# Kernel tuning notes

Hardware: AMD Instinct MI355X
Metric: run time of the kernel (lower is better)

## Reference

```python
import jax, jax.numpy as jnp
import numpy as np

D_IN = 1024
D_OUT = 1024


def setup_inputs() -> dict:
    key = jax.random.key(0)
    kx, kq, kk, kv = jax.random.split(key, 4)
    x = jax.random.normal(kx, (4, 2048, D_IN), dtype=jnp.float32)
    # nn.Linear weight has shape [d_out, d_in]; y = x @ W.T
    s = 1.0 / np.sqrt(D_IN)
    W_query = jax.random.uniform(kq, (D_OUT, D_IN), jnp.float32, -s, s)
    W_key = jax.random.uniform(kk, (D_OUT, D_IN), jnp.float32, -s, s)
    W_value = jax.random.uniform(kv, (D_OUT, D_IN), jnp.float32, -s, s)
    return {"x": x, "W_query": W_query, "W_key": W_key, "W_value": W_value}


def reference(x, W_query, W_key, W_value):
    # x: [b, n, d_in]; W_*: [d_out, d_in]
    q = jnp.einsum("bnd,kd->bnk", x, W_query)
    k = jnp.einsum("bnd,kd->bnk", x, W_key)
    v = jnp.einsum("bnd,kd->bnk", x, W_value)
    d_k = W_query.shape[0]
    scores = jnp.einsum("bqk,bnk->bqn", q, k) * (d_k ** -0.5)  # [b, n, n]
    weights = jax.nn.softmax(scores, axis=-1)
    return jnp.einsum("bqn,bnk->bqk", weights, v)
```

## Files before the change

kernel.cpp:

```cpp
#include <hip/hip_runtime.h>
#include <hip/hip_bf16.h>
#include <stdint.h>


typedef __attribute__((ext_vector_type(8))) short bf16x8;
typedef __attribute__((ext_vector_type(4))) float f32x4;

__device__ __forceinline__ void async_copy16(const void* g, void* l) {
  __builtin_amdgcn_global_load_lds(
      (__attribute__((address_space(1))) void*)(g),
      (__attribute__((address_space(3))) void*)(l),
      16, 0, 0);
}

template<int NI, int NT, int KS>
__device__ __forceinline__ void mainloop256(
    const __hip_bfloat16* __restrict__ aS,
    const __hip_bfloat16* __restrict__ bS,
    __hip_bfloat16* As, __hip_bfloat16* Bs,
    const int wid, const int wm, const int wn,
    const int l16, const int quad, const int sw,
    f32x4 (&acc)[8][NI])
{
  constexpr int NI2 = NI / 2;
  const bf16x8* Av = (const bf16x8*)As;
  const bf16x8* Bv = (const bf16x8*)Bs;
  char* lA = (char*)As + wid * 1024;
  char* lB = (char*)Bs + wid * 1024;
  bf16x8 bfr[NI][2];
  bf16x8 afc[2][2], afn[2][2];

#define SB0 __builtin_amdgcn_sched_barrier(0)

#define STG_A2(t) do { \
    _Pragma("unroll") \
    for (int p = 0; p < 4; ++p) \
      async_copy16(aS + ((t)*64 + (long long)p * 64 * KS), \
                   lA + ((t)&1)*32768 + p * 64 * 128); \
  } while (0)
#define STG_B2(t) do { \
    _Pragma("unroll") \
    for (int p = 0; p < NI; ++p) \
      async_copy16(bS + ((t)*64 + (long long)p * 64 * KS), \
                   lB + ((t)&1)*(NI*8192) + p * 64 * 128); \
  } while (0)

#define RD_AF(dst, t, phi) do { \
    _Pragma("unroll") \
    for (int m2 = 0; m2 < 2; ++m2) \
      _Pragma("unroll") \
      for (int kk = 0; kk < 2; ++kk) \
        dst[m2][kk] = Av[((t)&1)*2048 + (wm + ((phi)*2 + m2)*16 + l16)*8 + ((kk*4 + quad) ^ sw)]; \
  } while (0)
#define RD_BF(t, nlo, nhi) do { \
    _Pragma("unroll") \
    for (int ni = (nlo); ni < (nhi); ++ni) \
      _Pragma("unroll") \
      for (int kk = 0; kk < 2; ++kk) \
        bfr[ni][kk] = Bv[((t)&1)*(NI*512) + (wn + ni*16 + l16)*8 + ((kk*4 + quad) ^ sw)]; \
  } while (0)
#define MM(src, phi, nlo, nhi) do { \
    _Pragma("unroll") \
    for (int kk = 0; kk < 2; ++kk) \
      _Pragma("unroll") \
      for (int m2 = 0; m2 < 2; ++m2) \
        _Pragma("unroll") \
        for (int ni = (nlo); ni < (nhi); ++ni) \
          acc[(phi)*2 + m2][ni] = __builtin_amdgcn_mfma_f32_16x16x32_bf16( \
              src[m2][kk], bfr[ni][kk], acc[(phi)*2 + m2][ni], 0, 0, 0); \
  } while (0)

#define TILE(t, STG0_STMT, STG1_STMT, GATE_STMT) do { \
     \
    RD_BF(t, 0, NI2); \
    RD_AF(afc, t, 0); \
    STG0_STMT; \
    asm volatile("s_waitcnt lgkmcnt(0)"); SB0; \
    RD_BF(t, NI2, NI); \
    SB0; \
    RD_AF(afn, t, 1); \
    SB0; \
    __builtin_amdgcn_s_setprio(1); MM(afc, 0, 0, NI2); __builtin_amdgcn_s_setprio(0); \
    asm volatile("s_waitcnt lgkmcnt(4)"); SB0; \
    __builtin_amdgcn_s_setprio(1); MM(afc, 0, NI2, NI); __builtin_amdgcn_s_setprio(0); \
    SB0; \
    __builtin_amdgcn_s_barrier();    \
     \
    STG1_STMT; \
    asm volatile("s_waitcnt lgkmcnt(0)"); SB0; \
    RD_AF(afc, t, 2); \
    SB0; \
    __builtin_amdgcn_s_setprio(1); MM(afn, 1, 0, NI); __builtin_amdgcn_s_setprio(0); \
     \
    asm volatile("s_waitcnt lgkmcnt(0)"); SB0; \
    RD_AF(afn, t, 3); \
    SB0; \
    __builtin_amdgcn_s_setprio(1); MM(afc, 2, 0, NI); __builtin_amdgcn_s_setprio(0); \
     \
    asm volatile("s_waitcnt lgkmcnt(0)"); SB0; \
    __builtin_amdgcn_s_setprio(1); MM(afn, 3, 0, NI); __builtin_amdgcn_s_setprio(0); \
    GATE_STMT; \
    SB0; \
    __builtin_amdgcn_s_barrier(); \
  } while (0)

#define GATEN do { if constexpr (NI == 4) asm volatile("s_waitcnt vmcnt(4)"); \
                   else                   asm volatile("s_waitcnt vmcnt(2)"); } while (0)
#define GATE0 asm volatile("s_waitcnt vmcnt(0)")
#define GNONE (void)0

  STG_B2(0); STG_A2(0); STG_B2(1);
  GATEN;
  __builtin_amdgcn_s_barrier();

  #pragma unroll 1
  for (int i = 0; i < NT / 2 - 1; ++i) {
    const int ta = 2 * i, tb = 2 * i + 1;
    TILE(ta, STG_A2(tb),     STG_B2(ta + 2), GATEN);
    TILE(tb, STG_A2(ta + 2), STG_B2(tb + 2), GATEN);
  }
  TILE(NT - 2, STG_A2(NT - 1), GNONE, GATE0);
  TILE(NT - 1, GNONE,          GNONE, GNONE);

#undef TILE
#undef GATEN
#undef GATE0
#undef GNONE
#undef MM
#undef RD_BF
#undef RD_AF
#undef STG_A2
#undef STG_B2
#undef SB0
}

__global__ __launch_bounds__(512, 2)
void gemm_qk(const __hip_bfloat16* __restrict__ A,
             const __hip_bfloat16* __restrict__ B,
             __hip_bfloat16* __restrict__ Q,
             __hip_bfloat16* __restrict__ Kk)
{
  __shared__ __align__(16) __hip_bfloat16 As[2][256 * 64];
  __shared__ __align__(16) __hip_bfloat16 Bs[2][256 * 64];

  const int bid = blockIdx.x;
  const int s   = (bid & 7) * 32 + (bid >> 3);
  const long long tile_m = (long long)(s >> 3) * 256;
  const long long tile_n = (long long)(s & 7) * 256;

  const int tid  = threadIdx.x;
  const int wid  = tid >> 6;
  const int lane = tid & 63;
  const int srow = wid * 8 + (lane >> 3);
  const int scol = ((lane & 7) ^ (lane >> 3)) * 8;

  const __hip_bfloat16* aS = A + (tile_m + srow) * 1024 + scol;
  const __hip_bfloat16* bS = B + (tile_n + srow) * 1024 + scol;

  const int wm   = (wid >> 2) * 128;
  const int wn   = (wid & 3) * 64;
  const int quad = lane >> 4;
  const int l16  = lane & 15;
  const int sw   = l16 & 7;

  f32x4 acc[8][4];
  #pragma unroll
  for (int mi = 0; mi < 8; ++mi)
    #pragma unroll
    for (int ni = 0; ni < 4; ++ni)
      acc[mi][ni] = (f32x4){0.f, 0.f, 0.f, 0.f};

  mainloop256<4, 16, 1024>(aS, bS, &As[0][0], &Bs[0][0],
                           wid, wm, wn, l16, quad, sw, acc);

  const int mat = (int)(tile_n >> 10);
  __hip_bfloat16* outp = (mat == 0) ? Q : Kk;
  const float scale = (mat == 0) ? 0.03125f : 1.0f;
  const int coln0 = (int)(tile_n & 1023);
  #pragma unroll
  for (int mi = 0; mi < 8; ++mi) {
    #pragma unroll
    for (int r = 0; r < 4; ++r) {
      const long long row = tile_m + wm + mi * 16 + quad * 4 + r;
      #pragma unroll
      for (int ni = 0; ni < 4; ++ni) {
        const int col = coln0 + wn + ni * 16 + l16;
        outp[row * 1024 + col] = __float2bfloat16(acc[mi][ni][r] * scale);
      }
    }
  }
}

__global__ __launch_bounds__(512, 2)
void gemm_v(const __hip_bfloat16* __restrict__ A,
            const __hip_bfloat16* __restrict__ B,
            __hip_bfloat16* __restrict__ Vt)
{
  __shared__ __align__(16) __hip_bfloat16 As[2][256 * 64];
  __shared__ __align__(16) __hip_bfloat16 Bs[2][128 * 64];

  const int bid = blockIdx.x;
  const int s   = (bid & 7) * 32 + (bid >> 3);
  const long long tile_m = (long long)(s >> 3) * 256;
  const long long tile_n = (long long)(s & 7) * 128;

  const int tid  = threadIdx.x;
  const int wid  = tid >> 6;
  const int lane = tid & 63;
  const int srow = wid * 8 + (lane >> 3);
  const int scol = ((lane & 7) ^ (lane >> 3)) * 8;

  const __hip_bfloat16* aS = A + (tile_m + srow) * 1024 + scol;
  const __hip_bfloat16* bS = B + (tile_n + srow) * 1024 + scol;

  const int wm   = (wid >> 2) * 128;
  const int wn   = (wid & 3) * 32;
  const int quad = lane >> 4;
  const int l16  = lane & 15;
  const int sw   = l16 & 7;

  f32x4 acc[8][2];
  #pragma unroll
  for (int mi = 0; mi < 8; ++mi)
    #pragma unroll
    for (int ni = 0; ni < 2; ++ni)
      acc[mi][ni] = (f32x4){0.f, 0.f, 0.f, 0.f};

  mainloop256<2, 16, 1024>(aS, bS, &As[0][0], &Bs[0][0],
                           wid, wm, wn, l16, quad, sw, acc);

  const int b    = (int)(tile_m >> 11);
  const int seq0 = (int)(tile_m & 2047);
  const int d0   = (int)tile_n;
  #pragma unroll
  for (int mi = 0; mi < 8; ++mi) {
    const int seq = seq0 + wm + mi * 16 + quad * 4;
    #pragma unroll
    for (int ni = 0; ni < 2; ++ni) {
      const int d = d0 + wn + ni * 16 + l16;
      union { ushort4 u; unsigned short sh[4]; } pk;
      #pragma unroll
      for (int r = 0; r < 4; ++r)
        pk.sh[r] = __bfloat16_as_ushort(__float2bfloat16(acc[mi][ni][r]));
      *(ushort4*)(Vt + ((long long)(b * 1024 + d)) * 2048 + seq) = pk.u;
    }
  }
}

__global__ __launch_bounds__(512, 2)
void gemm_s_exp(const __hip_bfloat16* __restrict__ A,
                const __hip_bfloat16* __restrict__ B,
                __hip_bfloat16* __restrict__ Cout,
                float* __restrict__ part)
{
  __shared__ __align__(16) __hip_bfloat16 As[2][256 * 64];
  __shared__ __align__(16) __hip_bfloat16 Bs[2][256 * 64];

  const int bz = blockIdx.z;
  A += (long long)bz * 2048 * 1024;
  B += (long long)bz * 2048 * 1024;

  const long long tile_m = (long long)blockIdx.y * 256;
  const long long tile_n = (long long)blockIdx.x * 256;

  const int tid  = threadIdx.x;
  const int wid  = tid >> 6;
  const int lane = tid & 63;
  const int srow = wid * 8 + (lane >> 3);
  const int scol = ((lane & 7) ^ (lane >> 3)) * 8;

  const __hip_bfloat16* aS = A + (tile_m + srow) * 1024 + scol;
  const __hip_bfloat16* bS = B + (tile_n + srow) * 1024 + scol;

  const int wm   = (wid >> 2) * 128;
  const int wn   = (wid & 3) * 64;
  const int quad = lane >> 4;
  const int l16  = lane & 15;
  const int sw   = l16 & 7;

  f32x4 acc[8][4];
  #pragma unroll
  for (int mi = 0; mi < 8; ++mi)
    #pragma unroll
    for (int ni = 0; ni < 4; ++ni)
      acc[mi][ni] = (f32x4){0.f, 0.f, 0.f, 0.f};

  mainloop256<4, 16, 1024>(aS, bS, &As[0][0], &Bs[0][0],
                           wid, wm, wn, l16, quad, sw, acc);

  __hip_bfloat16* C = Cout + (long long)bz * 2048 * 2048;
  #pragma unroll
  for (int mi = 0; mi < 8; ++mi) {
    #pragma unroll
    for (int r = 0; r < 4; ++r) {
      const long long row = tile_m + wm + mi * 16 + quad * 4 + r;
      float ssum = 0.f;
      #pragma unroll
      for (int ni = 0; ni < 4; ++ni) {
        const float e = __expf(acc[mi][ni][r]);
        const __hip_bfloat16 h = __float2bfloat16(e);
        C[row * 2048 + tile_n + wn + ni * 16 + l16] = h;
        ssum += __bfloat162float(h);
      }
      #pragma unroll
      for (int off = 1; off < 16; off <<= 1) ssum += __shfl_xor(ssum, off, 64);
      if (l16 == 0)
        part[((long long)bz * 2048 + row) * 32 + blockIdx.x * 4 + (wid & 3)] = ssum;
    }
  }
}

__global__ __launch_bounds__(512, 2)
void gemm_pv(const __hip_bfloat16* __restrict__ A,
             const __hip_bfloat16* __restrict__ B,
             const float* __restrict__ part,
             float* __restrict__ Cout)
{
  __shared__ __align__(16) __hip_bfloat16 As[2][256 * 64];
  __shared__ __align__(16) __hip_bfloat16 Bs[2][128 * 64];
  __shared__ float rinv[256];

  const int bz = blockIdx.z;
  A += (long long)bz * 2048 * 2048;
  B += (long long)bz * 1024 * 2048;

  const long long tile_m = (long long)blockIdx.y * 256;
  const long long tile_n = (long long)blockIdx.x * 128;

  const int tid  = threadIdx.x;
  const int wid  = tid >> 6;
  const int lane = tid & 63;
  const int srow = wid * 8 + (lane >> 3);
  const int scol = ((lane & 7) ^ (lane >> 3)) * 8;

  const __hip_bfloat16* aS = A + (tile_m + srow) * 2048 + scol;
  const __hip_bfloat16* bS = B + (tile_n + srow) * 2048 + scol;

  const int wm   = (wid >> 2) * 128;
  const int wn   = (wid & 3) * 32;
  const int quad = lane >> 4;
  const int l16  = lane & 15;
  const int sw   = l16 & 7;

  f32x4 acc[8][2];
  #pragma unroll
  for (int mi = 0; mi < 8; ++mi)
    #pragma unroll
    for (int ni = 0; ni < 2; ++ni)
      acc[mi][ni] = (f32x4){0.f, 0.f, 0.f, 0.f};

  mainloop256<2, 32, 2048>(aS, bS, &As[0][0], &Bs[0][0],
                           wid, wm, wn, l16, quad, sw, acc);

  if (tid < 256) {
    const float4* pp = (const float4*)(part + ((long long)bz * 2048 + tile_m + tid) * 32);
    float s = 0.f;
    #pragma unroll
    for (int j = 0; j < 8; ++j) {
      const float4 f = pp[j];
      s += f.x + f.y + f.z + f.w;
    }
    rinv[tid] = 1.f / s;
  }
  __syncthreads();

  float* C = Cout + (long long)bz * 2048 * 1024;
  #pragma unroll
  for (int mi = 0; mi < 8; ++mi) {
    #pragma unroll
    for (int r = 0; r < 4; ++r) {
      const int rloc = wm + mi * 16 + quad * 4 + r;
      const float inv = rinv[rloc];
      const long long row = tile_m + rloc;
      #pragma unroll
      for (int ni = 0; ni < 2; ++ni) {
        const long long col = tile_n + wn + ni * 16 + l16;
        C[row * 1024 + col] = acc[mi][ni][r] * inv;
      }
    }
  }
}

__global__ __launch_bounds__(256)
void cast_all(const float* __restrict__ x,
              const float* __restrict__ Wq, const float* __restrict__ Wk,
              const float* __restrict__ Wv,
              __hip_bfloat16* __restrict__ xb, __hip_bfloat16* __restrict__ wcat)
{
  const int bx = blockIdx.x;
  const float* src;
  __hip_bfloat16* dst;
  int i;
  if (bx < 8192) {
    src = x; dst = xb; i = bx * 256 + threadIdx.x;
  } else {
    const int which = (bx - 8192) >> 10;
    src = (which == 0) ? Wq : (which == 1) ? Wk : Wv;
    dst = wcat + (long long)which * 1048576;
    i = ((bx - 8192) & 1023) * 256 + threadIdx.x;
  }
  const float4 f = ((const float4*)src)[i];
  union { ushort4 u; __hip_bfloat16 h[4]; } r;
  r.h[0] = __float2bfloat16(f.x);
  r.h[1] = __float2bfloat16(f.y);
  r.h[2] = __float2bfloat16(f.z);
  r.h[3] = __float2bfloat16(f.w);
  ((ushort4*)dst)[i] = r.u;
}

extern "C" void kernel_launch(void* const* d_in, const int* in_sizes, int n_in,
                              void* d_out, int out_size, void* d_ws, size_t ws_size,
                              hipStream_t stream)
{
  (void)in_sizes; (void)n_in; (void)out_size; (void)ws_size;

  const float* x  = (const float*)d_in[0];
  const float* Wq = (const float*)d_in[1];
  const float* Wk = (const float*)d_in[2];
  const float* Wv = (const float*)d_in[3];
  float* out = (float*)d_out;

  char* ws = (char*)d_ws;
  __hip_bfloat16* xb   = (__hip_bfloat16*)(ws);
  float*          part = (float*)(ws);
  __hip_bfloat16* wcat = (__hip_bfloat16*)(ws + (16LL << 20));
  __hip_bfloat16* Q    = (__hip_bfloat16*)(ws + (22LL << 20));
  __hip_bfloat16* Kk   = (__hip_bfloat16*)(ws + (38LL << 20));
  __hip_bfloat16* Vt   = (__hip_bfloat16*)(ws + (54LL << 20));
  __hip_bfloat16* S    = (__hip_bfloat16*)(ws + (70LL << 20));

  cast_all<<<11264, 256, 0, stream>>>(x, Wq, Wk, Wv, xb, wcat);

  gemm_qk<<<256, 512, 0, stream>>>(xb, wcat, Q, Kk);

  gemm_v<<<256, 512, 0, stream>>>(xb, wcat + 2097152, Vt);

  gemm_s_exp<<<dim3(8, 8, 4), 512, 0, stream>>>(Q, Kk, S, part);

  gemm_pv<<<dim3(8, 8, 4), 512, 0, stream>>>(S, Vt, part, out);
}
```

Before: 234.3 us.

## Remap blocks to XCDs for L2 locality and simplify LDS read/MFMA schedule

```diff
diff --git a/kernel.cpp b/kernel.cpp
--- a/kernel.cpp
+++ b/kernel.cpp
@@ -22,7 +22,6 @@
     const int l16, const int quad, const int sw,
     f32x4 (&acc)[8][NI])
 {
-  constexpr int NI2 = NI / 2;
   const bf16x8* Av = (const bf16x8*)As;
   const bf16x8* Bv = (const bf16x8*)Bs;
   char* lA = (char*)As + wid * 1024;
@@ -70,44 +69,38 @@
               src[m2][kk], bfr[ni][kk], acc[(phi)*2 + m2][ni], 0, 0, 0); \
   } while (0)
 
+#define GATEN do { SB0; \
+    if constexpr (NI == 4) asm volatile("s_waitcnt vmcnt(4)" ::: "memory"); \
+    else                   asm volatile("s_waitcnt vmcnt(2)" ::: "memory"); \
+  } while (0)
+#define GATE0 do { SB0; \
+    asm volatile("s_waitcnt vmcnt(0)" ::: "memory"); } while (0)
+#define GNONE (void)0
+
 #define TILE(t, STG0_STMT, STG1_STMT, GATE_STMT) do { \
      \
-    RD_BF(t, 0, NI2); \
+    RD_BF(t, 0, NI); \
     RD_AF(afc, t, 0); \
+    RD_AF(afn, t, 1); \
     STG0_STMT; \
-    asm volatile("s_waitcnt lgkmcnt(0)"); SB0; \
-    RD_BF(t, NI2, NI); \
-    SB0; \
-    RD_AF(afn, t, 1); \
-    SB0; \
-    __builtin_amdgcn_s_setprio(1); MM(afc, 0, 0, NI2); __builtin_amdgcn_s_setprio(0); \
-    asm volatile("s_waitcnt lgkmcnt(4)"); SB0; \
-    __builtin_amdgcn_s_setprio(1); MM(afc, 0, NI2, NI); __builtin_amdgcn_s_setprio(0); \
+    __builtin_amdgcn_s_setprio(1); MM(afc, 0, 0, NI); __builtin_amdgcn_s_setprio(0); \
     SB0; \
     __builtin_amdgcn_s_barrier();    \
      \
     STG1_STMT; \
-    asm volatile("s_waitcnt lgkmcnt(0)"); SB0; \
     RD_AF(afc, t, 2); \
-    SB0; \
-    __builtin_amdgcn_s_setprio(1); MM(afn, 1, 0, NI); __builtin_amdgcn_s_setprio(0); \
-     \
-    asm volatile("s_waitcnt lgkmcnt(0)"); SB0; \
+    __builtin_amdgcn_s_setprio(1); \
+    MM(afn, 1, 0, NI); \
+    __builtin_amdgcn_s_setprio(0); \
     RD_AF(afn, t, 3); \
-    SB0; \
-    __builtin_amdgcn_s_setprio(1); MM(afc, 2, 0, NI); __builtin_amdgcn_s_setprio(0); \
-     \
-    asm volatile("s_waitcnt lgkmcnt(0)"); SB0; \
-    __builtin_amdgcn_s_setprio(1); MM(afn, 3, 0, NI); __builtin_amdgcn_s_setprio(0); \
+    __builtin_amdgcn_s_setprio(1); \
+    MM(afc, 2, 0, NI); \
+    MM(afn, 3, 0, NI); \
+    __builtin_amdgcn_s_setprio(0); \
     GATE_STMT; \
     SB0; \
     __builtin_amdgcn_s_barrier(); \
   } while (0)
-
-#define GATEN do { if constexpr (NI == 4) asm volatile("s_waitcnt vmcnt(4)"); \
-                   else                   asm volatile("s_waitcnt vmcnt(2)"); } while (0)
-#define GATE0 asm volatile("s_waitcnt vmcnt(0)")
-#define GNONE (void)0
 
   STG_B2(0); STG_A2(0); STG_B2(1);
   GATEN;
@@ -256,12 +249,18 @@
   __shared__ __align__(16) __hip_bfloat16 As[2][256 * 64];
   __shared__ __align__(16) __hip_bfloat16 Bs[2][256 * 64];
 
-  const int bz = blockIdx.z;
+  const int u   = blockIdx.x + (blockIdx.y << 3) + (blockIdx.z << 6);
+  const int xcd = u & 7;
+  const int rr  = u >> 3;
+  const int bz  = xcd >> 1;
+  const int tmi = ((xcd & 1) << 2) + (rr >> 3);
+  const int tni = rr & 7;
+
   A += (long long)bz * 2048 * 1024;
   B += (long long)bz * 2048 * 1024;
 
-  const long long tile_m = (long long)blockIdx.y * 256;
-  const long long tile_n = (long long)blockIdx.x * 256;
+  const long long tile_m = (long long)tmi * 256;
+  const long long tile_n = (long long)tni * 256;
 
   const int tid  = threadIdx.x;
   const int wid  = tid >> 6;
@@ -305,7 +304,7 @@
       #pragma unroll
       for (int off = 1; off < 16; off <<= 1) ssum += __shfl_xor(ssum, off, 64);
       if (l16 == 0)
-        part[((long long)bz * 2048 + row) * 32 + blockIdx.x * 4 + (wid & 3)] = ssum;
+        part[((long long)bz * 2048 + row) * 32 + tni * 4 + (wid & 3)] = ssum;
     }
   }
 }
@@ -320,12 +319,18 @@
   __shared__ __align__(16) __hip_bfloat16 Bs[2][128 * 64];
   __shared__ float rinv[256];
 
-  const int bz = blockIdx.z;
+  const int u   = blockIdx.x + (blockIdx.y << 3) + (blockIdx.z << 6);
+  const int xcd = u & 7;
+  const int rr  = u >> 3;
+  const int bz  = xcd >> 1;
+  const int tmi = ((xcd & 1) << 2) + (rr >> 3);
+  const int tni = rr & 7;
+
   A += (long long)bz * 2048 * 2048;
   B += (long long)bz * 1024 * 2048;
 
-  const long long tile_m = (long long)blockIdx.y * 256;
-  const long long tile_n = (long long)blockIdx.x * 128;
+  const long long tile_m = (long long)tmi * 256;
+  const long long tile_n = (long long)tni * 128;
 
   const int tid  = threadIdx.x;
   const int wid  = tid >> 6;
```

Measured after the change: 222.2 us. 1.05x faster.
